# Kernel tuning notes

Measured on AMD Instinct MI355X. Metric: run time of the kernel, lower is better.

Reference implementation:

```python
import jax, jax.numpy as jnp
import numpy as np
import math

FEATURE_DIM = 1024
NUM_HEADS = 16
HEAD_SIZE = FEATURE_DIM // NUM_HEADS


def setup_inputs() -> dict:
    key = jax.random.key(0)
    ks = jax.random.split(key, 5)
    B, T, C = 4, 2048, FEATURE_DIM
    scale = 1.0 / math.sqrt(C)
    x = jax.random.normal(ks[0], (B, T, C), dtype=jnp.float32)
    # attention_proj: Linear(C, 3C) -> weight (3C, C), bias (3C,)
    W_qkv = jax.random.uniform(ks[1], (3 * C, C), jnp.float32, -scale, scale)
    b_qkv = jax.random.uniform(ks[2], (3 * C,), jnp.float32, -scale, scale)
    # final_proj: Linear(C, C)
    W_out = jax.random.uniform(ks[3], (C, C), jnp.float32, -scale, scale)
    b_out = jax.random.uniform(ks[4], (C,), jnp.float32, -scale, scale)
    return {"x": x, "W_qkv": W_qkv, "b_qkv": b_qkv, "W_out": W_out, "b_out": b_out}


def reference(x, W_qkv, b_qkv, W_out, b_out):
    B, T, C = x.shape
    H, hs = NUM_HEADS, HEAD_SIZE
    qkv = x @ W_qkv.T + b_qkv                     # (B, T, 3C)
    qkv = qkv.reshape(B, T, H, 3 * hs)            # per-head interleaved q|k|v
    q = qkv[..., :hs]                             # (B, T, H, hs)
    k = qkv[..., hs:2 * hs]
    v = qkv[..., 2 * hs:]
    att = jnp.einsum('bthd,bshd->bhts', q, k) / math.sqrt(hs)  # (B, H, T, T)
    att_prob = jax.nn.softmax(att, axis=-1)
    att_v = jnp.einsum('bhts,bshd->bthd', att_prob, v)         # (B, T, H, hs)
    att_v = att_v.reshape(B, T, C)
    return att_v @ W_out.T + b_out
```

## Files before the change

### kernel.cpp

```cpp
#include <hip/hip_runtime.h>
#include <hip/hip_bf16.h>


typedef unsigned short u16;
typedef short bf16x8 __attribute__((ext_vector_type(8)));
typedef float floatx4 __attribute__((ext_vector_type(4)));

#define BB 4
#define TT 2048
#define CC 1024
#define HH 16
#define CEXP 0.18033688f

#if __has_builtin(__builtin_amdgcn_exp2f)
#define EXP2(x) __builtin_amdgcn_exp2f(x)
#else
#define EXP2(x) exp2f(x)
#endif

__device__ __forceinline__ u16 f2bf(float f) {
    __hip_bfloat16 h = __float2bfloat16(f);
    u16 r; __builtin_memcpy(&r, &h, 2); return r;
}
__device__ __forceinline__ unsigned pkbf(float lo, float hi) {
    __hip_bfloat162 h2 = __float22bfloat162_rn(float2{lo, hi});
    unsigned r; __builtin_memcpy(&r, &h2, 4); return r;
}
__device__ __forceinline__ bf16x8 cvt8(const float* p) {
    floatx4 a = *(const floatx4*)p;
    floatx4 b = *(const floatx4*)(p + 4);
    bf16x8 r;
    r[0] = (short)f2bf(a[0]); r[1] = (short)f2bf(a[1]);
    r[2] = (short)f2bf(a[2]); r[3] = (short)f2bf(a[3]);
    r[4] = (short)f2bf(b[0]); r[5] = (short)f2bf(b[1]);
    r[6] = (short)f2bf(b[2]); r[7] = (short)f2bf(b[3]);
    return r;
}
__device__ __forceinline__ int sw8(int row, int slot) {
    return row * 64 + (((slot ^ (row & 7)) & 7) << 3);
}
__device__ __forceinline__ void gll16(const u16* g, u16* l) {
    __builtin_amdgcn_global_load_lds(
        (const __attribute__((address_space(1))) unsigned*)g,
        (__attribute__((address_space(3))) unsigned*)l, 16, 0, 0);
}

__device__ __forceinline__ void pl32swap(unsigned& a, unsigned& b) {
#if __has_builtin(__builtin_amdgcn_permlane32_swap)
    typedef unsigned u32x2 __attribute__((ext_vector_type(2)));
    u32x2 r = __builtin_amdgcn_permlane32_swap(a, b, false, false);
    a = r[0]; b = r[1];
#else
    const bool up = (threadIdx.x & 32) != 0;
    unsigned as = (unsigned)__shfl_xor((int)a, 32);
    unsigned bs = (unsigned)__shfl_xor((int)b, 32);
    unsigned na = up ? bs : a;
    unsigned nb = up ? b : as;
    a = na; b = nb;
#endif
}
__device__ __forceinline__ void pl16swap(unsigned& a, unsigned& b) {
#if __has_builtin(__builtin_amdgcn_permlane16_swap)
    typedef unsigned u32x2 __attribute__((ext_vector_type(2)));
    u32x2 r = __builtin_amdgcn_permlane16_swap(a, b, false, false);
    a = r[0]; b = r[1];
#else
    const bool up = (threadIdx.x & 16) != 0;
    unsigned as = (unsigned)__shfl_xor((int)a, 16);
    unsigned bs = (unsigned)__shfl_xor((int)b, 16);
    unsigned na = up ? bs : a;
    unsigned nb = up ? b : as;
    a = na; b = nb;
#endif
}

__global__ __launch_bounds__(256) void cvt_all(const float* __restrict__ x,
                                               const float* __restrict__ wq,
                                               const float* __restrict__ wo,
                                               u16* __restrict__ xb,
                                               u16* __restrict__ wqb,
                                               u16* __restrict__ wob) {
    const int nx8 = 8388608 / 8, nq8 = 3145728 / 8, no8 = 1048576 / 8;
    const int n8 = nx8 + nq8 + no8;
    for (int i = blockIdx.x * blockDim.x + threadIdx.x; i < n8;
         i += gridDim.x * blockDim.x) {
        const float* src;
        u16* dst;
        if (i < nx8)            { src = x  + (size_t)i * 8;          dst = xb  + (size_t)i * 8; }
        else if (i < nx8 + nq8) { size_t j = i - nx8; src = wq + j * 8; dst = wqb + j * 8; }
        else                    { size_t j = i - nx8 - nq8; src = wo + j * 8; dst = wob + j * 8; }
        floatx4 a = *(const floatx4*)src;
        floatx4 b = *(const floatx4*)(src + 4);
        union { bf16x8 v; unsigned u[4]; } r;
        r.u[0] = pkbf(a[0], a[1]); r.u[1] = pkbf(a[2], a[3]);
        r.u[2] = pkbf(b[0], b[1]); r.u[3] = pkbf(b[2], b[3]);
        *(bf16x8*)dst = r.v;
    }
}

template <int SCATTER, int QSLOT>
__global__ __launch_bounds__(256) void gemm_lds(const u16* __restrict__ Ab,
                                                const u16* __restrict__ Bb,
                                                const float* __restrict__ bias,
                                                void* __restrict__ Cv,
                                                int K, int N) {
    __shared__ u16 As[2][128 * 64];
    __shared__ u16 Bs[2][128 * 64];

    const int tid  = threadIdx.x;
    const int lane = tid & 63;
    const int wave = tid >> 6;
    const int quad = lane >> 4;
    const int l15  = lane & 15;
    const int wm   = (wave >> 1) * 64;
    const int wn   = (wave & 1) * 64;
    const int blockM = blockIdx.y * 128;
    const int blockN = blockIdx.x * 128;

    floatx4 acc[4][4];
#pragma unroll
    for (int i = 0; i < 4; i++)
#pragma unroll
        for (int j = 0; j < 4; j++) acc[i][j] = (floatx4){0.f, 0.f, 0.f, 0.f};

    const int lr = lane >> 3;
    const int scol = ((lane & 7) ^ (lr & 7)) * 8;

    auto stage = [&](int buf, int k0) {
#pragma unroll
        for (int i = 0; i < 4; i++) {
            const int c = wave * 4 + i;
            const int row = blockM + c * 8 + lr;
            const u16* src;
            if (QSLOT) {
                const int b = row >> 11, t = row & 2047, h = k0 >> 6;
                src = Ab + ((size_t)((b * HH + h) * TT + t)) * 192 + scol;
            } else {
                src = Ab + (size_t)row * K + k0 + scol;
            }
            gll16(src, &As[buf][c * 512]);
        }
#pragma unroll
        for (int i = 0; i < 4; i++) {
            const int c = wave * 4 + i;
            const int row = blockN + c * 8 + lr;
            gll16(Bb + (size_t)row * K + k0 + scol, &Bs[buf][c * 512]);
        }
    };

    stage(0, 0);
    __syncthreads();

    int cur = 0;
    for (int k0 = 0; k0 < K; k0 += 64) {
        if (k0 + 64 < K) stage(cur ^ 1, k0 + 64);

#pragma unroll
        for (int ks = 0; ks < 2; ks++) {
            const int slot = ks * 4 + quad;
            bf16x8 af[4], bfr[4];
#pragma unroll
            for (int mi = 0; mi < 4; mi++)
                af[mi] = *(const bf16x8*)&As[cur][sw8(wm + mi * 16 + l15, slot)];
#pragma unroll
            for (int ni = 0; ni < 4; ni++)
                bfr[ni] = *(const bf16x8*)&Bs[cur][sw8(wn + ni * 16 + l15, slot)];
#pragma unroll
            for (int mi = 0; mi < 4; mi++)
#pragma unroll
                for (int ni = 0; ni < 4; ni++)
                    acc[mi][ni] = __builtin_amdgcn_mfma_f32_16x16x32_bf16(
                        af[mi], bfr[ni], acc[mi][ni], 0, 0, 0);
        }

        __syncthreads();
        cur ^= 1;
    }

#pragma unroll
    for (int ni = 0; ni < 4; ni++) {
        const int col = blockN + wn + ni * 16 + l15;
        const float bv = bias[col];
        if (SCATTER) {
            const int h = col / 192;
            const int r = col - h * 192;
            const float qs = (r < 64) ? CEXP : 1.0f;
            u16* C = (u16*)Cv;
#pragma unroll
            for (int mi = 0; mi < 4; mi++)
#pragma unroll
                for (int reg = 0; reg < 4; reg++) {
                    const int row = blockM + wm + mi * 16 + quad * 4 + reg;
                    const int b = row >> 11, t = row & 2047;
                    C[((size_t)((b * HH + h) * TT + t)) * 192 + r] =
                        f2bf((acc[mi][ni][reg] + bv) * qs);
                }
        } else {
            float* C = (float*)Cv;
#pragma unroll
            for (int mi = 0; mi < 4; mi++)
#pragma unroll
                for (int reg = 0; reg < 4; reg++) {
                    const int row = blockM + wm + mi * 16 + quad * 4 + reg;
                    C[(size_t)row * N + col] = acc[mi][ni][reg] + bv;
                }
        }
    }
}

template <int SCATTER, int QSLOT>
__global__ __launch_bounds__(256) void gemm_bt(const void* __restrict__ Av,
                                               const float* __restrict__ Bw,
                                               const float* __restrict__ bias,
                                               void* __restrict__ Cv,
                                               int K, int N) {
    __shared__ u16 As[128 * 64];
    __shared__ u16 Bs[128 * 64];

    const int tid  = threadIdx.x;
    const int lane = tid & 63;
    const int wave = tid >> 6;
    const int quad = lane >> 4;
    const int l15  = lane & 15;
    const int wm   = (wave >> 1) * 64;
    const int wn   = (wave & 1) * 64;
    const int blockM = blockIdx.y * 128;
    const int blockN = blockIdx.x * 128;

    floatx4 acc[4][4];
#pragma unroll
    for (int i = 0; i < 4; i++)
#pragma unroll
        for (int j = 0; j < 4; j++) acc[i][j] = (floatx4){0.f, 0.f, 0.f, 0.f};

    const int srow = lane >> 3;
    const int scol = (lane & 7) * 8;

    for (int k0 = 0; k0 < K; k0 += 64) {
        bf16x8 at[4], bt[4];
#pragma unroll
        for (int i = 0; i < 4; i++) {
            const int row = blockM + (i * 4 + wave) * 8 + srow;
            if (QSLOT) {
                const int b = row >> 11, t = row & 2047, h = k0 >> 6;
                at[i] = *(const bf16x8*)((const u16*)Av
                         + ((size_t)((b * HH + h) * TT + t)) * 192 + scol);
            } else {
                at[i] = cvt8((const float*)Av + (size_t)row * K + k0 + scol);
            }
        }
#pragma unroll
        for (int i = 0; i < 4; i++)
            bt[i] = cvt8(Bw + (size_t)(blockN + (i * 4 + wave) * 8 + srow) * K + k0 + scol);

        __syncthreads();
#pragma unroll
        for (int i = 0; i < 4; i++)
            *(bf16x8*)&As[sw8((i * 4 + wave) * 8 + srow, lane & 7)] = at[i];
#pragma unroll
        for (int i = 0; i < 4; i++)
            *(bf16x8*)&Bs[sw8((i * 4 + wave) * 8 + srow, lane & 7)] = bt[i];
        __syncthreads();

#pragma unroll
        for (int ks = 0; ks < 2; ks++) {
            const int slot = ks * 4 + quad;
            bf16x8 af[4], bfr[4];
#pragma unroll
            for (int mi = 0; mi < 4; mi++)
                af[mi] = *(const bf16x8*)&As[sw8(wm + mi * 16 + l15, slot)];
#pragma unroll
            for (int ni = 0; ni < 4; ni++)
                bfr[ni] = *(const bf16x8*)&Bs[sw8(wn + ni * 16 + l15, slot)];
#pragma unroll
            for (int mi = 0; mi < 4; mi++)
#pragma unroll
                for (int ni = 0; ni < 4; ni++)
                    acc[mi][ni] = __builtin_amdgcn_mfma_f32_16x16x32_bf16(
                        af[mi], bfr[ni], acc[mi][ni], 0, 0, 0);
        }
    }

#pragma unroll
    for (int ni = 0; ni < 4; ni++) {
        const int col = blockN + wn + ni * 16 + l15;
        const float bv = bias[col];
        if (SCATTER) {
            const int h = col / 192;
            const int r = col - h * 192;
            const float qs = (r < 64) ? CEXP : 1.0f;
            u16* C = (u16*)Cv;
#pragma unroll
            for (int mi = 0; mi < 4; mi++)
#pragma unroll
                for (int reg = 0; reg < 4; reg++) {
                    const int row = blockM + wm + mi * 16 + quad * 4 + reg;
                    const int b = row >> 11, t = row & 2047;
                    C[((size_t)((b * HH + h) * TT + t)) * 192 + r] =
                        f2bf((acc[mi][ni][reg] + bv) * qs);
                }
        } else {
            float* C = (float*)Cv;
#pragma unroll
            for (int mi = 0; mi < 4; mi++)
#pragma unroll
                for (int reg = 0; reg < 4; reg++) {
                    const int row = blockM + wm + mi * 16 + quad * 4 + reg;
                    C[(size_t)row * N + col] = acc[mi][ni][reg] + bv;
                }
        }
    }
}

__global__ __launch_bounds__(512) void attn_fwd(u16* __restrict__ qkv,
                                                u16* __restrict__ avd) {
    __shared__ u16 Ks[64 * 64];
    __shared__ u16 Vts[64 * 64];

    const int tid  = threadIdx.x;
    const int lane = tid & 63;
    const int wave = tid >> 6;
    const int quad = lane >> 4;
    const int l15  = lane & 15;

    const int bh = blockIdx.y;
    const int t0 = blockIdx.x * 256;
    u16* Qg = qkv + (size_t)bh * TT * 192;

    bf16x8 qf[2][2];
#pragma unroll
    for (int qi = 0; qi < 2; qi++) {
        const int trow = t0 + wave * 32 + qi * 16 + l15;
#pragma unroll
        for (int ks = 0; ks < 2; ks++)
            qf[qi][ks] = *(const bf16x8*)(Qg + (size_t)trow * 192 + ks * 32 + quad * 8);
    }

    bf16x8 ones;
#pragma unroll
    for (int j = 0; j < 8; j++) ones[j] = (short)0x3F80;
    const floatx4 zero4 = (floatx4){0.f, 0.f, 0.f, 0.f};

    floatx4 o[2][4];
#pragma unroll
    for (int qi = 0; qi < 2; qi++)
#pragma unroll
        for (int di = 0; di < 4; di++) o[qi][di] = (floatx4){0.f, 0.f, 0.f, 0.f};
    floatx4 l_acc[2] = {(floatx4){0.f,0.f,0.f,0.f}, (floatx4){0.f,0.f,0.f,0.f}};

    const int lr = lane >> 3;
    const int scolsw = ((lane & 7) ^ (lr & 7)) * 8;
    const int vs  = tid & 63;
    const int vd0 = (tid >> 6) * 8;

    for (int s0 = 0; s0 < TT; s0 += 64) {
        bf16x8 v0 = *(const bf16x8*)(Qg + (size_t)(s0 + vs) * 192 + 128 + vd0);

        __syncthreads();
        gll16(Qg + (size_t)(s0 + wave * 8 + lr) * 192 + 64 + scolsw,
              &Ks[wave * 512]);
        {
            const int vslot = vs >> 3, voff = vs & 7;
#pragma unroll
            for (int j = 0; j < 8; j++) {
                const int row = vd0 + j;
                Vts[row * 64 + (((vslot ^ (row & 7)) & 7) << 3) + voff] = (u16)v0[j];
            }
        }
        __syncthreads();

        floatx4 s_acc[4][2];
        __builtin_amdgcn_s_setprio(1);
        {
            bf16x8 kf[4];
#pragma unroll
            for (int si = 0; si < 4; si++)
                kf[si] = *(const bf16x8*)&Ks[sw8(si * 16 + l15, quad)];
#pragma unroll
            for (int si = 0; si < 4; si++)
#pragma unroll
                for (int qi = 0; qi < 2; qi++)
                    s_acc[si][qi] = __builtin_amdgcn_mfma_f32_16x16x32_bf16(
                        kf[si], qf[qi][0], zero4, 0, 0, 0);
        }
        {
            bf16x8 kf[4];
#pragma unroll
            for (int si = 0; si < 4; si++)
                kf[si] = *(const bf16x8*)&Ks[sw8(si * 16 + l15, 4 + quad)];
#pragma unroll
            for (int si = 0; si < 4; si++)
#pragma unroll
                for (int qi = 0; qi < 2; qi++)
                    s_acc[si][qi] = __builtin_amdgcn_mfma_f32_16x16x32_bf16(
                        kf[si], qf[qi][1], s_acc[si][qi], 0, 0, 0);
        }
        __builtin_amdgcn_s_setprio(0);

        unsigned c[4][2][2];
#pragma unroll
        for (int si = 0; si < 4; si++)
#pragma unroll
            for (int qi = 0; qi < 2; qi++) {
                floatx4 p;
#pragma unroll
                for (int r = 0; r < 4; r++) p[r] = EXP2(s_acc[si][qi][r]);
                c[si][qi][0] = pkbf(p[0], p[1]);
                c[si][qi][1] = pkbf(p[2], p[3]);
            }

        union PF { bf16x8 v; unsigned u[4]; } pf[2][2];
#pragma unroll
        for (int qi = 0; qi < 2; qi++)
#pragma unroll
            for (int ks = 0; ks < 2; ks++)
#pragma unroll
                for (int h = 0; h < 2; h++) {
                    unsigned a = c[2 * ks][qi][h];
                    unsigned b = c[2 * ks + 1][qi][h];
                    pl32swap(a, b);
                    pl16swap(a, b);
                    pf[qi][ks].u[h]     = a;
                    pf[qi][ks].u[2 + h] = b;
                }

        __builtin_amdgcn_s_setprio(1);
#pragma unroll
        for (int ks = 0; ks < 2; ks++) {
            const int slot = ks * 4 + quad;
            bf16x8 vf[4];
#pragma unroll
            for (int di = 0; di < 4; di++)
                vf[di] = *(const bf16x8*)&Vts[sw8(di * 16 + l15, slot)];
#pragma unroll
            for (int qi = 0; qi < 2; qi++) {
#pragma unroll
                for (int di = 0; di < 4; di++)
                    o[qi][di] = __builtin_amdgcn_mfma_f32_16x16x32_bf16(
                        pf[qi][ks].v, vf[di], o[qi][di], 0, 0, 0);
                l_acc[qi] = __builtin_amdgcn_mfma_f32_16x16x32_bf16(
                    pf[qi][ks].v, ones, l_acc[qi], 0, 0, 0);
            }
        }
        __builtin_amdgcn_s_setprio(0);
    }

    if (avd) {
        const int b = bh >> 4, h = bh & 15;
        u16* D = avd + (size_t)b * TT * CC + h * 64;
#pragma unroll
        for (int qi = 0; qi < 2; qi++)
#pragma unroll
            for (int reg = 0; reg < 4; reg++) {
                const float inv_l = 1.0f / l_acc[qi][reg];
                const int trow = t0 + wave * 32 + qi * 16 + quad * 4 + reg;
#pragma unroll
                for (int di = 0; di < 4; di++)
                    D[(size_t)trow * CC + di * 16 + l15] = f2bf(o[qi][di][reg] * inv_l);
            }
    } else {
#pragma unroll
        for (int qi = 0; qi < 2; qi++)
#pragma unroll
            for (int reg = 0; reg < 4; reg++) {
                const float inv_l = 1.0f / l_acc[qi][reg];
                const int trow = t0 + wave * 32 + qi * 16 + quad * 4 + reg;
#pragma unroll
                for (int di = 0; di < 4; di++)
                    Qg[(size_t)trow * 192 + di * 16 + l15] = f2bf(o[qi][di][reg] * inv_l);
            }
    }
}

extern "C" void kernel_launch(void* const* d_in, const int* in_sizes, int n_in,
                              void* d_out, int out_size, void* d_ws, size_t ws_size,
                              hipStream_t stream) {
    (void)out_size;
    float* out = (float*)d_out;

    const float *x = nullptr, *wq = nullptr, *bq = nullptr, *wo = nullptr, *bo = nullptr;
    int found = 0;
    for (int i = 0; i < n_in && i < 8; i++) {
        switch (in_sizes[i]) {
            case 8388608: x  = (const float*)d_in[i]; found |= 1;  break;
            case 3145728: wq = (const float*)d_in[i]; found |= 2;  break;
            case 3072:    bq = (const float*)d_in[i]; found |= 4;  break;
            case 1048576: wo = (const float*)d_in[i]; found |= 8;  break;
            case 1024:    bo = (const float*)d_in[i]; found |= 16; break;
        }
    }
    if (found != 31) {
        x  = (const float*)d_in[0]; wq = (const float*)d_in[1];
        bq = (const float*)d_in[2]; wo = (const float*)d_in[3];
        bo = (const float*)d_in[4];
    }

    u16* qkv = (u16*)d_ws;

    const dim3 g1(3 * CC / 128, BB * TT / 128), ga(TT / 256, BB * HH),
               g3(CC / 128, BB * TT / 128);

    if (ws_size >= 92274688u) {
        u16* xb  = qkv + 25165824;
        u16* wqb = qkv + 33554432;
        u16* wob = qkv + 36700160;
        u16* avd = qkv + 37748736;
        cvt_all<<<2048, 256, 0, stream>>>(x, wq, wo, xb, wqb, wob);
        gemm_lds<1, 0><<<g1, 256, 0, stream>>>(xb, wqb, bq, qkv, CC, 3 * CC);
        attn_fwd<<<ga, 512, 0, stream>>>(qkv, avd);
        gemm_lds<0, 0><<<g3, 256, 0, stream>>>(avd, wob, bo, out, CC, CC);
    } else if (ws_size >= 75497472u) {
        u16* xb  = qkv + 25165824;
        u16* wqb = qkv + 33554432;
        u16* wob = qkv + 36700160;
        cvt_all<<<2048, 256, 0, stream>>>(x, wq, wo, xb, wqb, wob);
        gemm_lds<1, 0><<<g1, 256, 0, stream>>>(xb, wqb, bq, qkv, CC, 3 * CC);
        attn_fwd<<<ga, 512, 0, stream>>>(qkv, nullptr);
        gemm_lds<0, 1><<<g3, 256, 0, stream>>>(qkv, wob, bo, out, CC, CC);
    } else {
        gemm_bt<1, 0><<<g1, 256, 0, stream>>>(x, wq, bq, qkv, CC, 3 * CC);
        attn_fwd<<<ga, 512, 0, stream>>>(qkv, nullptr);
        gemm_bt<0, 1><<<g3, 256, 0, stream>>>(qkv, wo, bo, out, CC, CC);
    }
}
```

Measured before the change: 261.1 us.

## Write V transposed from QKV GEMM epilogue and load it directly into LDS

The QKV projection epilogue now writes the V part in a transposed (b,h,d,t) buffer when workspace allows. The attention kernel then loads V tiles into LDS with direct global-to-LDS copies instead of doing a per-element register transpose into LDS. The attention output is written back into the Q slot and the output GEMM reads it from there (QSLOT=1), replacing the separate dense buffer. The transposed V stores in the GEMM epilogue are strided across t, so they may coalesce poorly, which trades cost inside the attention loop for scattered writes in the GEMM.

```diff
diff --git a/kernel.cpp b/kernel.cpp
--- a/kernel.cpp
+++ b/kernel.cpp
@@ -103,7 +103,8 @@
                                                 const u16* __restrict__ Bb,
                                                 const float* __restrict__ bias,
                                                 void* __restrict__ Cv,
-                                                int K, int N) {
+                                                int K, int N,
+                                                u16* __restrict__ Vt) {
     __shared__ u16 As[2][128 * 64];
     __shared__ u16 Bs[2][128 * 64];
 
@@ -184,17 +185,30 @@
         if (SCATTER) {
             const int h = col / 192;
             const int r = col - h * 192;
-            const float qs = (r < 64) ? CEXP : 1.0f;
             u16* C = (u16*)Cv;
-#pragma unroll
-            for (int mi = 0; mi < 4; mi++)
-#pragma unroll
-                for (int reg = 0; reg < 4; reg++) {
-                    const int row = blockM + wm + mi * 16 + quad * 4 + reg;
-                    const int b = row >> 11, t = row & 2047;
-                    C[((size_t)((b * HH + h) * TT + t)) * 192 + r] =
-                        f2bf((acc[mi][ni][reg] + bv) * qs);
-                }
+            if (Vt && r >= 128) {
+                const int d = r - 128;
+#pragma unroll
+                for (int mi = 0; mi < 4; mi++)
+#pragma unroll
+                    for (int reg = 0; reg < 4; reg++) {
+                        const int row = blockM + wm + mi * 16 + quad * 4 + reg;
+                        const int b = row >> 11, t = row & 2047;
+                        Vt[((size_t)(b * HH + h) * 64 + d) * TT + t] =
+                            f2bf(acc[mi][ni][reg] + bv);
+                    }
+            } else {
+                const float qs = (r < 64) ? CEXP : 1.0f;
+#pragma unroll
+                for (int mi = 0; mi < 4; mi++)
+#pragma unroll
+                    for (int reg = 0; reg < 4; reg++) {
+                        const int row = blockM + wm + mi * 16 + quad * 4 + reg;
+                        const int b = row >> 11, t = row & 2047;
+                        C[((size_t)((b * HH + h) * TT + t)) * 192 + r] =
+                            f2bf((acc[mi][ni][reg] + bv) * qs);
+                    }
+            }
         } else {
             float* C = (float*)Cv;
 #pragma unroll
@@ -313,7 +327,7 @@
 }
 
 __global__ __launch_bounds__(512) void attn_fwd(u16* __restrict__ qkv,
-                                                u16* __restrict__ avd) {
+                                                const u16* __restrict__ Vt) {
     __shared__ u16 Ks[64 * 64];
     __shared__ u16 Vts[64 * 64];
 
@@ -326,6 +340,7 @@
     const int bh = blockIdx.y;
     const int t0 = blockIdx.x * 256;
     u16* Qg = qkv + (size_t)bh * TT * 192;
+    const u16* VtB = Vt ? Vt + (size_t)bh * 64 * TT : nullptr;
 
     bf16x8 qf[2][2];
 #pragma unroll
@@ -354,12 +369,17 @@
     const int vd0 = (tid >> 6) * 8;
 
     for (int s0 = 0; s0 < TT; s0 += 64) {
-        bf16x8 v0 = *(const bf16x8*)(Qg + (size_t)(s0 + vs) * 192 + 128 + vd0);
+        bf16x8 v0;
+        if (!Vt)
+            v0 = *(const bf16x8*)(Qg + (size_t)(s0 + vs) * 192 + 128 + vd0);
 
         __syncthreads();
         gll16(Qg + (size_t)(s0 + wave * 8 + lr) * 192 + 64 + scolsw,
               &Ks[wave * 512]);
-        {
+        if (Vt) {
+            gll16(VtB + (size_t)(wave * 8 + lr) * TT + s0 + scolsw,
+                  &Vts[wave * 512]);
+        } else {
             const int vslot = vs >> 3, voff = vs & 7;
 #pragma unroll
             for (int j = 0; j < 8; j++) {
@@ -445,31 +465,16 @@
         __builtin_amdgcn_s_setprio(0);
     }
 
-    if (avd) {
-        const int b = bh >> 4, h = bh & 15;
-        u16* D = avd + (size_t)b * TT * CC + h * 64;
-#pragma unroll
-        for (int qi = 0; qi < 2; qi++)
-#pragma unroll
-            for (int reg = 0; reg < 4; reg++) {
-                const float inv_l = 1.0f / l_acc[qi][reg];
-                const int trow = t0 + wave * 32 + qi * 16 + quad * 4 + reg;
-#pragma unroll
-                for (int di = 0; di < 4; di++)
-                    D[(size_t)trow * CC + di * 16 + l15] = f2bf(o[qi][di][reg] * inv_l);
-            }
-    } else {
-#pragma unroll
-        for (int qi = 0; qi < 2; qi++)
-#pragma unroll
-            for (int reg = 0; reg < 4; reg++) {
-                const float inv_l = 1.0f / l_acc[qi][reg];
-                const int trow = t0 + wave * 32 + qi * 16 + quad * 4 + reg;
-#pragma unroll
-                for (int di = 0; di < 4; di++)
-                    Qg[(size_t)trow * 192 + di * 16 + l15] = f2bf(o[qi][di][reg] * inv_l);
-            }
-    }
+#pragma unroll
+    for (int qi = 0; qi < 2; qi++)
+#pragma unroll
+        for (int reg = 0; reg < 4; reg++) {
+            const float inv_l = 1.0f / l_acc[qi][reg];
+            const int trow = t0 + wave * 32 + qi * 16 + quad * 4 + reg;
+#pragma unroll
+            for (int di = 0; di < 4; di++)
+                Qg[(size_t)trow * 192 + di * 16 + l15] = f2bf(o[qi][di][reg] * inv_l);
+        }
 }
 
 extern "C" void kernel_launch(void* const* d_in, const int* in_sizes, int n_in,
@@ -504,19 +509,19 @@
         u16* xb  = qkv + 25165824;
         u16* wqb = qkv + 33554432;
         u16* wob = qkv + 36700160;
-        u16* avd = qkv + 37748736;
+        u16* Vt  = qkv + 37748736;
         cvt_all<<<2048, 256, 0, stream>>>(x, wq, wo, xb, wqb, wob);
-        gemm_lds<1, 0><<<g1, 256, 0, stream>>>(xb, wqb, bq, qkv, CC, 3 * CC);
-        attn_fwd<<<ga, 512, 0, stream>>>(qkv, avd);
-        gemm_lds<0, 0><<<g3, 256, 0, stream>>>(avd, wob, bo, out, CC, CC);
+        gemm_lds<1, 0><<<g1, 256, 0, stream>>>(xb, wqb, bq, qkv, CC, 3 * CC, Vt);
+        attn_fwd<<<ga, 512, 0, stream>>>(qkv, Vt);
+        gemm_lds<0, 1><<<g3, 256, 0, stream>>>(qkv, wob, bo, out, CC, CC, nullptr);
     } else if (ws_size >= 75497472u) {
         u16* xb  = qkv + 25165824;
         u16* wqb = qkv + 33554432;
         u16* wob = qkv + 36700160;
         cvt_all<<<2048, 256, 0, stream>>>(x, wq, wo, xb, wqb, wob);
-        gemm_lds<1, 0><<<g1, 256, 0, stream>>>(xb, wqb, bq, qkv, CC, 3 * CC);
+        gemm_lds<1, 0><<<g1, 256, 0, stream>>>(xb, wqb, bq, qkv, CC, 3 * CC, nullptr);
         attn_fwd<<<ga, 512, 0, stream>>>(qkv, nullptr);
-        gemm_lds<0, 1><<<g3, 256, 0, stream>>>(qkv, wob, bo, out, CC, CC);
+        gemm_lds<0, 1><<<g3, 256, 0, stream>>>(qkv, wob, bo, out, CC, CC, nullptr);
     } else {
         gemm_bt<1, 0><<<g1, 256, 0, stream>>>(x, wq, bq, qkv, CC, 3 * CC);
         attn_fwd<<<ga, 512, 0, stream>>>(qkv, nullptr);
```

After: 271.5 us. 1.04x slower.
